# Kernel tuning notes

Measured on AMD Instinct MI355X. Metric: run time of the kernel, lower is better.

## Reference

```python
import jax, jax.numpy as jnp
import numpy as np

HIDDEN = 2048
SEL = 512
RES = HIDDEN - SEL
YSZ = 2048
RANK = 64
EPS = 1e-5


def _layernorm(x, gamma, beta):
    mu = jnp.mean(x, axis=-1, keepdims=True)
    var = jnp.mean(jnp.square(x - mu), axis=-1, keepdims=True)
    return (x - mu) * jax.lax.rsqrt(var + EPS) * gamma + beta


def setup_inputs() -> dict:
    key = jax.random.key(0)
    ks = jax.random.split(key, 8)
    B, S = 4, 4096
    hidden_states = jax.random.normal(ks[0], (B, S, HIDDEN), dtype=jnp.float32)
    y = jax.random.normal(ks[1], (B, S, YSZ), dtype=jnp.float32)
    A = -jnp.ones((1, 1, SEL), dtype=jnp.float32) + 0.02 * jax.random.normal(ks[2], (1, 1, SEL), dtype=jnp.float32)
    W_w = jax.random.normal(ks[3], (HIDDEN, YSZ), dtype=jnp.float32) * (1.0 / np.sqrt(YSZ))
    dd_w = jax.random.normal(ks[4], (RANK, HIDDEN + YSZ), dtype=jnp.float32) * (1.0 / np.sqrt(HIDDEN + YSZ))
    du_w = jax.random.normal(ks[5], (SEL, RANK), dtype=jnp.float32) * (1.0 / np.sqrt(RANK))
    t = 0.001 + jax.random.uniform(ks[6], (SEL,), dtype=jnp.float32) * (0.1 - 0.001)
    du_b = jnp.log(jnp.expm1(t))
    sel_gamma = jnp.ones((SEL,), dtype=jnp.float32)
    sel_beta = jnp.zeros((SEL,), dtype=jnp.float32)
    res_gamma = jnp.ones((RES,), dtype=jnp.float32)
    res_beta = jnp.zeros((RES,), dtype=jnp.float32)
    return {"hidden_states": hidden_states, "y": y, "A": A, "W_w": W_w,
            "dd_w": dd_w, "du_w": du_w, "du_b": du_b,
            "sel_gamma": sel_gamma, "sel_beta": sel_beta,
            "res_gamma": res_gamma, "res_beta": res_beta}


def reference(hidden_states, y, A, W_w, dd_w, du_w, du_b,
              sel_gamma, sel_beta, res_gamma, res_beta):
    sel_h = hidden_states[..., :SEL]
    res_h = hidden_states[..., SEL:]
    # W(y) split
    wy = jnp.einsum('bsy,hy->bsh', y, W_w)
    sel_y, res_y = wy[..., :SEL], wy[..., SEL:]
    # split layernorm of hidden_states
    normed = jnp.concatenate([
        _layernorm(sel_h, sel_gamma, sel_beta),
        _layernorm(res_h, res_gamma, res_beta)], axis=-1)
    # low-rank delta path
    cat = jnp.concatenate([normed, y], axis=-1)  # [B,S,HIDDEN+YSZ]
    low = jnp.einsum('bsc,rc->bsr', cat, dd_w)   # [B,S,RANK]
    delta = jnp.einsum('bsr,dr->bsd', low, du_w) + du_b  # [B,S,SEL]
    delta = jax.nn.softplus(delta)
    A_neg = -jax.nn.softplus(A)                  # [1,1,SEL]
    A_bar = jnp.exp(delta * A_neg)
    B_bar = (A_bar - 1.0) / A_neg
    sel_out = A_bar * sel_h + B_bar * sel_y
    res_out = res_h + res_y
    return jnp.concatenate([sel_out, res_out], axis=-1)
```

## Files before the change

### kernel.cpp

```cpp
#include <hip/hip_runtime.h>
#include <hip/hip_bf16.h>
#include <stdint.h>

#define NTOK   16384
#define HID    2048
#define SELN   512
#define RESN   1536
#define YSZn   2048
#define RANKn  64
#define EPSf   1e-5f

typedef __bf16 bf16x8 __attribute__((ext_vector_type(8)));
typedef float f32x4 __attribute__((ext_vector_type(4)));

__device__ __forceinline__ unsigned short f2bf(float f) {
  unsigned u = __float_as_uint(f);
  u += 0x7fff + ((u >> 16) & 1);
  return (unsigned short)(u >> 16);
}
__device__ __forceinline__ float bf2f(unsigned short h) {
  return __uint_as_float(((unsigned)h) << 16);
}
__device__ __forceinline__ float softplus_f(float x) {
  return fmaxf(x, 0.f) + log1pf(expf(-fabsf(x)));
}

#define GLD16(gp, lp) __builtin_amdgcn_global_load_lds( \
    (const __attribute__((address_space(1))) void*)(gp), \
    (__attribute__((address_space(3))) void*)(lp), 16, 0, 0)

#define CY (NTOK * HID / 8)
#define CW (HID * YSZn / 8)
#define CD (RANKn * (HID + YSZn) / 8)
__global__ __launch_bounds__(256) void k_convert(
    const float* __restrict__ y, const float* __restrict__ Ww,
    const float* __restrict__ ddw,
    unsigned short* __restrict__ ybf, unsigned short* __restrict__ wbf,
    unsigned short* __restrict__ dbf) {
  int64_t stride = (int64_t)gridDim.x * blockDim.x;
  for (int64_t i = (int64_t)blockIdx.x * blockDim.x + threadIdx.x;
       i < CY + CW + CD; i += stride) {
    const float* src; unsigned short* dst;
    if (i < CY)            { src = y   + i * 8;            dst = ybf + i * 8; }
    else if (i < CY + CW)  { int64_t j = i - CY;       src = Ww  + j * 8; dst = wbf + j * 8; }
    else                   { int64_t j = i - CY - CW;  src = ddw + j * 8; dst = dbf + j * 8; }
    float4 a = ((const float4*)src)[0];
    float4 b = ((const float4*)src)[1];
    union { unsigned short u[8]; uint4 q; } o;
    o.u[0]=f2bf(a.x); o.u[1]=f2bf(a.y); o.u[2]=f2bf(a.z); o.u[3]=f2bf(a.w);
    o.u[4]=f2bf(b.x); o.u[5]=f2bf(b.y); o.u[6]=f2bf(b.z); o.u[7]=f2bf(b.w);
    *(uint4*)dst = o.q;
  }
}

__global__ __launch_bounds__(256) void k_gemm_wy(
    const unsigned short* __restrict__ Y,
    const unsigned short* __restrict__ W,
    unsigned short* __restrict__ wy) {
  __shared__ unsigned short As[128 * 32];
  __shared__ unsigned short Bs[128 * 32];
  int bid = blockIdx.x;
  int swz = (bid & 7) * 256 + (bid >> 3);
  int mt = swz & 127, nt = swz >> 7;
  int m0 = mt * 128, n0 = nt * 128;
  int tid = threadIdx.x, w = tid >> 6, l = tid & 63;
  int wr = w >> 1, wc = w & 1;
  f32x4 acc[4][4] = {};

  int off0 = w * 1024 + l * 16;
  int r0 = off0 >> 6, kb0 = off0 & 63;
  int off1 = off0 + 4096;
  int r1 = off1 >> 6, kb1 = off1 & 63;
  const char* Ab = (const char*)Y;
  const char* Bb = (const char*)W;

  for (int kt = 0; kt < 64; ++kt) {
    int k0 = kt * 32;
    GLD16(Ab + ((size_t)(m0 + r0) * HID + k0) * 2 + kb0, (char*)As + w * 1024);
    GLD16(Ab + ((size_t)(m0 + r1) * HID + k0) * 2 + kb1, (char*)As + w * 1024 + 4096);
    GLD16(Bb + ((size_t)(n0 + r0) * HID + k0) * 2 + kb0, (char*)Bs + w * 1024);
    GLD16(Bb + ((size_t)(n0 + r1) * HID + k0) * 2 + kb1, (char*)Bs + w * 1024 + 4096);
    __syncthreads();
    bf16x8 af[4], bv[4];
    #pragma unroll
    for (int mi = 0; mi < 4; ++mi) {
      int row = wr * 64 + mi * 16 + (l & 15);
      af[mi] = *reinterpret_cast<const bf16x8*>(&As[row * 32 + ((l >> 4) * 8)]);
    }
    #pragma unroll
    for (int ni = 0; ni < 4; ++ni) {
      int row = wc * 64 + ni * 16 + (l & 15);
      bv[ni] = *reinterpret_cast<const bf16x8*>(&Bs[row * 32 + ((l >> 4) * 8)]);
    }
    #pragma unroll
    for (int mi = 0; mi < 4; ++mi)
      #pragma unroll
      for (int ni = 0; ni < 4; ++ni)
        acc[mi][ni] = __builtin_amdgcn_mfma_f32_16x16x32_bf16(af[mi], bv[ni], acc[mi][ni], 0, 0, 0);
    if (kt < 63) __syncthreads();
  }
  #pragma unroll
  for (int mi = 0; mi < 4; ++mi)
    #pragma unroll
    for (int ni = 0; ni < 4; ++ni) {
      int row = m0 + wr * 64 + mi * 16 + ((l >> 4) * 4);
      int col = n0 + wc * 64 + ni * 16 + (l & 15);
      #pragma unroll
      for (int rg = 0; rg < 4; ++rg)
        wy[(size_t)(row + rg) * HID + col] = f2bf(acc[mi][ni][rg]);
    }
}

__global__ __launch_bounds__(256) void k_ln(
    const float* __restrict__ hidden,
    const float* __restrict__ sg, const float* __restrict__ sb,
    const float* __restrict__ rg, const float* __restrict__ rb,
    unsigned short* __restrict__ normed) {
  int tok = blockIdx.x, tid = threadIdx.x;
  const float* x = hidden + (size_t)tok * HID;
  float4 a = ((const float4*)x)[tid * 2];
  float4 b = ((const float4*)x)[tid * 2 + 1];
  float v[8] = {a.x, a.y, a.z, a.w, b.x, b.y, b.z, b.w};
  float s = 0.f, ss = 0.f;
  #pragma unroll
  for (int j = 0; j < 8; ++j) { s += v[j]; ss += v[j] * v[j]; }
  #pragma unroll
  for (int off = 32; off > 0; off >>= 1) {
    s  += __shfl_xor(s, off);
    ss += __shfl_xor(ss, off);
  }
  __shared__ float ps[4], pss[4];
  int w = tid >> 6;
  if ((tid & 63) == 0) { ps[w] = s; pss[w] = ss; }
  __syncthreads();
  float mu, rstd; const float* gam; const float* bet; int cb;
  if (tid < 64) {
    float S = ps[0], SS = pss[0];
    mu = S * (1.f / 512.f);
    rstd = rsqrtf(SS * (1.f / 512.f) - mu * mu + EPSf);
    gam = sg; bet = sb; cb = tid * 8;
  } else {
    float S = ps[1] + ps[2] + ps[3], SS = pss[1] + pss[2] + pss[3];
    mu = S * (1.f / 1536.f);
    rstd = rsqrtf(SS * (1.f / 1536.f) - mu * mu + EPSf);
    gam = rg; bet = rb; cb = tid * 8 - 512;
  }
  union { unsigned short u[8]; uint4 q; } o;
  #pragma unroll
  for (int j = 0; j < 8; ++j)
    o.u[j] = f2bf((v[j] - mu) * rstd * gam[cb + j] + bet[cb + j]);
  *(uint4*)&normed[(size_t)tok * HID + tid * 8] = o.q;
}

__global__ __launch_bounds__(256) void k_gemm_low(
    const unsigned short* __restrict__ normed,
    const unsigned short* __restrict__ ybf,
    const unsigned short* __restrict__ ddw,
    float* __restrict__ low) {
  __shared__ unsigned short As[64 * 64];
  __shared__ unsigned short Bs[64 * 64];
  int m0 = blockIdx.x * 64;
  int tid = threadIdx.x, w = tid >> 6, l = tid & 63;
  f32x4 acc[4] = {};
  int off0 = w * 1024 + l * 16;
  int r0 = off0 >> 7, kb0 = off0 & 127;
  int off1 = off0 + 4096;
  int r1 = off1 >> 7, kb1 = off1 & 127;

  for (int kt = 0; kt < 64; ++kt) {
    const char* Asrc = (const char*)((kt < 32) ? normed : ybf);
    int k0 = (kt & 31) * 64;
    GLD16(Asrc + ((size_t)(m0 + r0) * HID + k0) * 2 + kb0, (char*)As + w * 1024);
    GLD16(Asrc + ((size_t)(m0 + r1) * HID + k0) * 2 + kb1, (char*)As + w * 1024 + 4096);
    GLD16((const char*)ddw + ((size_t)r0 * 4096 + kt * 64) * 2 + kb0, (char*)Bs + w * 1024);
    GLD16((const char*)ddw + ((size_t)r1 * 4096 + kt * 64) * 2 + kb1, (char*)Bs + w * 1024 + 4096);
    __syncthreads();
    #pragma unroll
    for (int kk = 0; kk < 2; ++kk) {
      bf16x8 af = *reinterpret_cast<const bf16x8*>(
          &As[(w * 16 + (l & 15)) * 64 + kk * 32 + (l >> 4) * 8]);
      #pragma unroll
      for (int ni = 0; ni < 4; ++ni) {
        bf16x8 bv = *reinterpret_cast<const bf16x8*>(
            &Bs[(ni * 16 + (l & 15)) * 64 + kk * 32 + (l >> 4) * 8]);
        acc[ni] = __builtin_amdgcn_mfma_f32_16x16x32_bf16(af, bv, acc[ni], 0, 0, 0);
      }
    }
    if (kt < 63) __syncthreads();
  }
  #pragma unroll
  for (int ni = 0; ni < 4; ++ni) {
    int row = m0 + w * 16 + ((l >> 4) * 4);
    int col = ni * 16 + (l & 15);
    #pragma unroll
    for (int rg = 0; rg < 4; ++rg)
      low[(size_t)(row + rg) * 64 + col] = acc[ni][rg];
  }
}

__global__ __launch_bounds__(512) void k_final(
    const float* __restrict__ hidden,
    const unsigned short* __restrict__ wy,
    const float* __restrict__ low,
    const float* __restrict__ A,
    const float* __restrict__ duw,
    const float* __restrict__ dub,
    float* __restrict__ out) {
  __shared__ float slow[8][64];
  int t0 = blockIdx.x * 8;
  int tid = threadIdx.x;
  slow[tid >> 6][tid & 63] = low[(size_t)t0 * 64 + tid];
  __syncthreads();

  int d = tid;
  float aneg = -softplus_f(A[d]);
  float dubv = dub[d];
  float wrow[64];
  #pragma unroll
  for (int r4 = 0; r4 < 16; ++r4) {
    float4 t = *(const float4*)&duw[(size_t)d * 64 + r4 * 4];
    wrow[r4 * 4 + 0] = t.x; wrow[r4 * 4 + 1] = t.y;
    wrow[r4 * 4 + 2] = t.z; wrow[r4 * 4 + 3] = t.w;
  }
  #pragma unroll 1
  for (int tk = 0; tk < 8; ++tk) {
    float acc = dubv;
    #pragma unroll
    for (int r = 0; r < 64; ++r) acc += wrow[r] * slow[tk][r];
    float delta = softplus_f(acc);
    float abar = expf(delta * aneg);
    float bbar = (abar - 1.f) / aneg;
    size_t base = (size_t)(t0 + tk) * HID;
    float selh = hidden[base + d];
    float sely = bf2f(wy[base + d]);
    out[base + d] = abar * selh + bbar * sely;
  }
  for (int i = tid; i < 8 * 384; i += 512) {
    int tk = i / 384, j = i - tk * 384;
    size_t base = (size_t)(t0 + tk) * HID + 512 + (size_t)j * 4;
    float4 h4 = *(const float4*)&hidden[base];
    ushort4 w4 = *(const ushort4*)&wy[base];
    float4 o;
    o.x = h4.x + bf2f(w4.x);
    o.y = h4.y + bf2f(w4.y);
    o.z = h4.z + bf2f(w4.z);
    o.w = h4.w + bf2f(w4.w);
    *(float4*)&out[base] = o;
  }
}

extern "C" void kernel_launch(void* const* d_in, const int* in_sizes, int n_in,
                              void* d_out, int out_size, void* d_ws, size_t ws_size,
                              hipStream_t stream) {
  (void)in_sizes; (void)n_in; (void)out_size; (void)ws_size;
  const float* hidden = (const float*)d_in[0];
  const float* y      = (const float*)d_in[1];
  const float* A      = (const float*)d_in[2];
  const float* Ww     = (const float*)d_in[3];
  const float* ddw    = (const float*)d_in[4];
  const float* duw    = (const float*)d_in[5];
  const float* dub    = (const float*)d_in[6];
  const float* sg     = (const float*)d_in[7];
  const float* sb     = (const float*)d_in[8];
  const float* rg     = (const float*)d_in[9];
  const float* rb     = (const float*)d_in[10];
  float* out = (float*)d_out;
  char* ws = (char*)d_ws;
  unsigned short* ybf  = (unsigned short*)(ws);
  unsigned short* wbf  = (unsigned short*)(ws + 67108864);
  unsigned short* dbf  = (unsigned short*)(ws + 75497472);
  unsigned short* wybf = (unsigned short*)(ws + 76021760);
  unsigned short* nrm  = (unsigned short*)(ws + 143130624);
  float*          low  = (float*)(ws + 210239488);

  hipLaunchKernelGGL(k_convert,  dim3(2048),  dim3(256), 0, stream, y, Ww, ddw, ybf, wbf, dbf);
  hipLaunchKernelGGL(k_gemm_wy,  dim3(2048),  dim3(256), 0, stream, ybf, wbf, wybf);
  hipLaunchKernelGGL(k_ln,       dim3(16384), dim3(256), 0, stream, hidden, sg, sb, rg, rb, nrm);
  hipLaunchKernelGGL(k_gemm_low, dim3(256),   dim3(256), 0, stream, nrm, ybf, dbf, low);
  hipLaunchKernelGGL(k_final,    dim3(2048),  dim3(512), 0, stream, hidden, wybf, low, A, duw, dub, out);
}
```

Before: 691.3 us.

## Rewrite wy GEMM with 256x256 double-buffered tiles and fused residual epilogue

Replaces the main W(y) GEMM with 256x256 tiles on 512 threads, a 128KB double-buffered LDS pipeline with swizzled layout, explicit waitcnt/barrier scheduling and setprio around MFMA clusters. The residual half (columns 512+) is written directly as hidden + wy in fp32 in the GEMM epilogue, so only the selective 512 columns are stored as bf16. This removes the full bf16 wy round-trip and the residual pass in k_final. The low-rank GEMM also gets swizzled double-buffered staging. The cost is large LDS usage per block, which limits occupancy, plus subtle manual vmcnt accounting.

```diff
diff --git a/kernel.cpp b/kernel.cpp
--- a/kernel.cpp
+++ b/kernel.cpp
@@ -5,9 +5,7 @@
 #define NTOK   16384
 #define HID    2048
 #define SELN   512
-#define RESN   1536
 #define YSZn   2048
-#define RANKn  64
 #define EPSf   1e-5f
 
 typedef __bf16 bf16x8 __attribute__((ext_vector_type(8)));
@@ -28,10 +26,13 @@
 #define GLD16(gp, lp) __builtin_amdgcn_global_load_lds( \
     (const __attribute__((address_space(1))) void*)(gp), \
     (__attribute__((address_space(3))) void*)(lp), 16, 0, 0)
+#define BAR()  __builtin_amdgcn_s_barrier()
+#define PRIO1() __builtin_amdgcn_s_setprio(1)
+#define PRIO0() __builtin_amdgcn_s_setprio(0)
 
 #define CY (NTOK * HID / 8)
 #define CW (HID * YSZn / 8)
-#define CD (RANKn * (HID + YSZn) / 8)
+#define CD (64 * (HID + YSZn) / 8)
 __global__ __launch_bounds__(256) void k_convert(
     const float* __restrict__ y, const float* __restrict__ Ww,
     const float* __restrict__ ddw,
@@ -53,62 +54,163 @@
   }
 }
 
-__global__ __launch_bounds__(256) void k_gemm_wy(
+__global__ __launch_bounds__(512, 2) void k_gemm_wy(
     const unsigned short* __restrict__ Y,
     const unsigned short* __restrict__ W,
-    unsigned short* __restrict__ wy) {
-  __shared__ unsigned short As[128 * 32];
-  __shared__ unsigned short Bs[128 * 32];
+    const float* __restrict__ hidden,
+    unsigned short* __restrict__ wysel,
+    float* __restrict__ out) {
+  __shared__ char lds[131072];
   int bid = blockIdx.x;
-  int swz = (bid & 7) * 256 + (bid >> 3);
-  int mt = swz & 127, nt = swz >> 7;
-  int m0 = mt * 128, n0 = nt * 128;
-  int tid = threadIdx.x, w = tid >> 6, l = tid & 63;
-  int wr = w >> 1, wc = w & 1;
-  f32x4 acc[4][4] = {};
-
-  int off0 = w * 1024 + l * 16;
-  int r0 = off0 >> 6, kb0 = off0 & 63;
-  int off1 = off0 + 4096;
-  int r1 = off1 >> 6, kb1 = off1 & 63;
-  const char* Ab = (const char*)Y;
-  const char* Bb = (const char*)W;
-
-  for (int kt = 0; kt < 64; ++kt) {
-    int k0 = kt * 32;
-    GLD16(Ab + ((size_t)(m0 + r0) * HID + k0) * 2 + kb0, (char*)As + w * 1024);
-    GLD16(Ab + ((size_t)(m0 + r1) * HID + k0) * 2 + kb1, (char*)As + w * 1024 + 4096);
-    GLD16(Bb + ((size_t)(n0 + r0) * HID + k0) * 2 + kb0, (char*)Bs + w * 1024);
-    GLD16(Bb + ((size_t)(n0 + r1) * HID + k0) * 2 + kb1, (char*)Bs + w * 1024 + 4096);
-    __syncthreads();
+  int nt = bid & 7, mt = bid >> 3;
+  int m0 = mt * 256, n0 = nt * 256;
+  int tid = threadIdx.x;
+  int l = tid & 63, w = tid >> 6;
+  int wr = w >> 2, wc = w & 3;
+
+  int rowS[2], colS[2];
+  #pragma unroll
+  for (int i = 0; i < 2; ++i) {
+    int L  = i * 8192 + tid * 16;
+    int rb = L >> 10;
+    int b  = L & 1023;
+    int rr = (b >> 6) & 15;
+    int cb = (b & 63) ^ ((rr >> 3) << 5);
+    rowS[i] = rb * 16 + rr;
+    colS[i] = cb >> 1;
+  }
+  const unsigned short* aSrc0 = Y + (size_t)(m0 + rowS[0]) * HID + colS[0];
+  const unsigned short* aSrc1 = Y + (size_t)(m0 + rowS[1]) * HID + colS[1];
+  const unsigned short* bSrc0 = W + (size_t)(n0 + rowS[0]) * HID + colS[0];
+  const unsigned short* bSrc1 = W + (size_t)(n0 + rowS[1]) * HID + colS[1];
+
+  int inner = (((l & 15) * 64) + ((l >> 4) * 16)) ^ (((l >> 3) & 1) << 5);
+  const char* ldsp = (const char*)lds;
+
+  f32x4 acc[8][4] = {};
+
+#define STAGE_A(kt, kh, bb) do { \
+    GLD16(aSrc0 + (size_t)(kt) * 64 + (kh) * 32, lds + (bb) + (kh) * 16384 + w * 1024); \
+    GLD16(aSrc1 + (size_t)(kt) * 64 + (kh) * 32, lds + (bb) + (kh) * 16384 + 8192 + w * 1024); \
+  } while (0)
+#define STAGE_B(kt, kh, bb) do { \
+    GLD16(bSrc0 + (size_t)(kt) * 64 + (kh) * 32, lds + 65536 + (bb) + (kh) * 16384 + w * 1024); \
+    GLD16(bSrc1 + (size_t)(kt) * 64 + (kh) * 32, lds + 65536 + (bb) + (kh) * 16384 + 8192 + w * 1024); \
+  } while (0)
+
+  auto rdA = [&](int cbase, int kk, int mg, bf16x8* af) {
+    #pragma unroll
+    for (int mi = 0; mi < 4; ++mi)
+      af[mi] = *(const bf16x8*)(ldsp + cbase + kk * 16384 +
+                                (mg * 8 + wr * 4 + mi) * 1024 + inner);
+  };
+  auto rdB = [&](int cbase, int kk, bf16x8* bv) {
+    #pragma unroll
+    for (int ni = 0; ni < 4; ++ni)
+      bv[ni] = *(const bf16x8*)(ldsp + 65536 + cbase + kk * 16384 +
+                                (wc * 4 + ni) * 1024 + inner);
+  };
+
+  STAGE_A(0, 0, 0); STAGE_B(0, 0, 0); STAGE_A(0, 1, 0); STAGE_B(0, 1, 0);
+  asm volatile("s_waitcnt vmcnt(4)");
+  BAR();
+
+  int buf = 0;
+  for (int kt = 0; kt < 32; ++kt) {
+    int cb = buf * 32768;
+    int sb = 32768 - cb;
+    bool last = (kt == 31);
     bf16x8 af[4], bv[4];
-    #pragma unroll
-    for (int mi = 0; mi < 4; ++mi) {
-      int row = wr * 64 + mi * 16 + (l & 15);
-      af[mi] = *reinterpret_cast<const bf16x8*>(&As[row * 32 + ((l >> 4) * 8)]);
-    }
-    #pragma unroll
-    for (int ni = 0; ni < 4; ++ni) {
-      int row = wc * 64 + ni * 16 + (l & 15);
-      bv[ni] = *reinterpret_cast<const bf16x8*>(&Bs[row * 32 + ((l >> 4) * 8)]);
-    }
+
+    rdA(cb, 0, 0, af); rdB(cb, 0, bv);
+    if (!last) STAGE_A(kt + 1, 0, sb);
+    BAR();
+    asm volatile("s_waitcnt lgkmcnt(0)");
+    PRIO1();
     #pragma unroll
     for (int mi = 0; mi < 4; ++mi)
       #pragma unroll
       for (int ni = 0; ni < 4; ++ni)
         acc[mi][ni] = __builtin_amdgcn_mfma_f32_16x16x32_bf16(af[mi], bv[ni], acc[mi][ni], 0, 0, 0);
-    if (kt < 63) __syncthreads();
-  }
-  #pragma unroll
-  for (int mi = 0; mi < 4; ++mi)
-    #pragma unroll
-    for (int ni = 0; ni < 4; ++ni) {
-      int row = m0 + wr * 64 + mi * 16 + ((l >> 4) * 4);
-      int col = n0 + wc * 64 + ni * 16 + (l & 15);
-      #pragma unroll
-      for (int rg = 0; rg < 4; ++rg)
-        wy[(size_t)(row + rg) * HID + col] = f2bf(acc[mi][ni][rg]);
-    }
+    PRIO0();
+    BAR();
+
+    rdA(cb, 0, 1, af);
+    if (!last) STAGE_B(kt + 1, 0, sb);
+    BAR();
+    asm volatile("s_waitcnt lgkmcnt(0)");
+    PRIO1();
+    #pragma unroll
+    for (int mi = 0; mi < 4; ++mi)
+      #pragma unroll
+      for (int ni = 0; ni < 4; ++ni)
+        acc[4 + mi][ni] = __builtin_amdgcn_mfma_f32_16x16x32_bf16(af[mi], bv[ni], acc[4 + mi][ni], 0, 0, 0);
+    PRIO0();
+    if (last) asm volatile("s_waitcnt vmcnt(0)");
+    else      asm volatile("s_waitcnt vmcnt(4)");
+    BAR();
+
+    rdA(cb, 1, 0, af); rdB(cb, 1, bv);
+    if (!last) STAGE_A(kt + 1, 1, sb);
+    BAR();
+    asm volatile("s_waitcnt lgkmcnt(0)");
+    PRIO1();
+    #pragma unroll
+    for (int mi = 0; mi < 4; ++mi)
+      #pragma unroll
+      for (int ni = 0; ni < 4; ++ni)
+        acc[mi][ni] = __builtin_amdgcn_mfma_f32_16x16x32_bf16(af[mi], bv[ni], acc[mi][ni], 0, 0, 0);
+    PRIO0();
+    BAR();
+
+    rdA(cb, 1, 1, af);
+    if (!last) STAGE_B(kt + 1, 1, sb);
+    BAR();
+    asm volatile("s_waitcnt lgkmcnt(0)");
+    PRIO1();
+    #pragma unroll
+    for (int mi = 0; mi < 4; ++mi)
+      #pragma unroll
+      for (int ni = 0; ni < 4; ++ni)
+        acc[4 + mi][ni] = __builtin_amdgcn_mfma_f32_16x16x32_bf16(af[mi], bv[ni], acc[4 + mi][ni], 0, 0, 0);
+    PRIO0();
+    if (!last) asm volatile("s_waitcnt vmcnt(4)");
+    BAR();
+
+    buf ^= 1;
+  }
+
+  if (nt < 2) {
+    #pragma unroll
+    for (int mg = 0; mg < 2; ++mg)
+      #pragma unroll
+      for (int mi = 0; mi < 4; ++mi)
+        #pragma unroll
+        for (int ni = 0; ni < 4; ++ni) {
+          int row = m0 + mg * 128 + wr * 64 + mi * 16 + ((l >> 4) * 4);
+          int col = n0 + wc * 64 + ni * 16 + (l & 15);
+          #pragma unroll
+          for (int rg = 0; rg < 4; ++rg)
+            wysel[(size_t)(row + rg) * SELN + col] = f2bf(acc[mg * 4 + mi][ni][rg]);
+        }
+  } else {
+    #pragma unroll
+    for (int mg = 0; mg < 2; ++mg)
+      #pragma unroll
+      for (int mi = 0; mi < 4; ++mi)
+        #pragma unroll
+        for (int ni = 0; ni < 4; ++ni) {
+          int row = m0 + mg * 128 + wr * 64 + mi * 16 + ((l >> 4) * 4);
+          int col = n0 + wc * 64 + ni * 16 + (l & 15);
+          #pragma unroll
+          for (int rg = 0; rg < 4; ++rg) {
+            size_t idx = (size_t)(row + rg) * HID + col;
+            out[idx] = hidden[idx] + acc[mg * 4 + mi][ni][rg];
+          }
+        }
+  }
+#undef STAGE_A
+#undef STAGE_B
 }
 
 __global__ __launch_bounds__(256) void k_ln(
@@ -157,36 +259,54 @@
     const unsigned short* __restrict__ ybf,
     const unsigned short* __restrict__ ddw,
     float* __restrict__ low) {
-  __shared__ unsigned short As[64 * 64];
-  __shared__ unsigned short Bs[64 * 64];
+  __shared__ char lds[32768];
   int m0 = blockIdx.x * 64;
   int tid = threadIdx.x, w = tid >> 6, l = tid & 63;
   f32x4 acc[4] = {};
-  int off0 = w * 1024 + l * 16;
-  int r0 = off0 >> 7, kb0 = off0 & 127;
-  int off1 = off0 + 4096;
-  int r1 = off1 >> 7, kb1 = off1 & 127;
-
+
+  int rowS[2], colS[2];
+  #pragma unroll
+  for (int i = 0; i < 2; ++i) {
+    int L  = i * 4096 + tid * 16;
+    int sbt = L >> 10;
+    int b  = L & 1023;
+    int rr = (b >> 6) & 15;
+    rowS[i] = (sbt >> 1) * 16 + rr;
+    colS[i] = (sbt & 1) * 32 + (((b & 63) ^ ((rr >> 3) << 5)) >> 1);
+  }
+  int inner = (((l & 15) * 64) + ((l >> 4) * 16)) ^ (((l >> 3) & 1) << 5);
+  const char* ldsp = (const char*)lds;
+
+  auto stage = [&](const unsigned short* As_, int kt, int bb) {
+    int k0 = (kt & 31) * 64;
+    GLD16(As_ + (size_t)(m0 + rowS[0]) * HID + k0 + colS[0], lds + bb + w * 1024);
+    GLD16(As_ + (size_t)(m0 + rowS[1]) * HID + k0 + colS[1], lds + bb + 4096 + w * 1024);
+    GLD16(ddw + (size_t)rowS[0] * 4096 + kt * 64 + colS[0], lds + bb + 8192 + w * 1024);
+    GLD16(ddw + (size_t)rowS[1] * 4096 + kt * 64 + colS[1], lds + bb + 8192 + 4096 + w * 1024);
+  };
+
+  stage(normed, 0, 0);
+  asm volatile("s_waitcnt vmcnt(0)");
+  BAR();
+  int buf = 0;
   for (int kt = 0; kt < 64; ++kt) {
-    const char* Asrc = (const char*)((kt < 32) ? normed : ybf);
-    int k0 = (kt & 31) * 64;
-    GLD16(Asrc + ((size_t)(m0 + r0) * HID + k0) * 2 + kb0, (char*)As + w * 1024);
-    GLD16(Asrc + ((size_t)(m0 + r1) * HID + k0) * 2 + kb1, (char*)As + w * 1024 + 4096);
-    GLD16((const char*)ddw + ((size_t)r0 * 4096 + kt * 64) * 2 + kb0, (char*)Bs + w * 1024);
-    GLD16((const char*)ddw + ((size_t)r1 * 4096 + kt * 64) * 2 + kb1, (char*)Bs + w * 1024 + 4096);
-    __syncthreads();
-    #pragma unroll
-    for (int kk = 0; kk < 2; ++kk) {
-      bf16x8 af = *reinterpret_cast<const bf16x8*>(
-          &As[(w * 16 + (l & 15)) * 64 + kk * 32 + (l >> 4) * 8]);
-      #pragma unroll
-      for (int ni = 0; ni < 4; ++ni) {
-        bf16x8 bv = *reinterpret_cast<const bf16x8*>(
-            &Bs[(ni * 16 + (l & 15)) * 64 + kk * 32 + (l >> 4) * 8]);
-        acc[ni] = __builtin_amdgcn_mfma_f32_16x16x32_bf16(af, bv, acc[ni], 0, 0, 0);
-      }
+    int cb = buf * 16384, sb = 16384 - cb;
+    if (kt < 63) stage((kt + 1 < 32) ? normed : ybf, kt + 1, sb);
+    bf16x8 af0 = *(const bf16x8*)(ldsp + cb + (w * 2 + 0) * 1024 + inner);
+    bf16x8 af1 = *(const bf16x8*)(ldsp + cb + (w * 2 + 1) * 1024 + inner);
+    #pragma unroll
+    for (int ni = 0; ni < 4; ++ni) {
+      bf16x8 b0 = *(const bf16x8*)(ldsp + cb + 8192 + (ni * 2 + 0) * 1024 + inner);
+      acc[ni] = __builtin_amdgcn_mfma_f32_16x16x32_bf16(af0, b0, acc[ni], 0, 0, 0);
     }
-    if (kt < 63) __syncthreads();
+    #pragma unroll
+    for (int ni = 0; ni < 4; ++ni) {
+      bf16x8 b1 = *(const bf16x8*)(ldsp + cb + 8192 + (ni * 2 + 1) * 1024 + inner);
+      acc[ni] = __builtin_amdgcn_mfma_f32_16x16x32_bf16(af1, b1, acc[ni], 0, 0, 0);
+    }
+    if (kt < 63) asm volatile("s_waitcnt vmcnt(0)");
+    BAR();
+    buf ^= 1;
   }
   #pragma unroll
   for (int ni = 0; ni < 4; ++ni) {
@@ -200,7 +320,7 @@
 
 __global__ __launch_bounds__(512) void k_final(
     const float* __restrict__ hidden,
-    const unsigned short* __restrict__ wy,
+    const unsigned short* __restrict__ wysel,
     const float* __restrict__ low,
     const float* __restrict__ A,
     const float* __restrict__ duw,
@@ -230,22 +350,10 @@
     float delta = softplus_f(acc);
     float abar = expf(delta * aneg);
     float bbar = (abar - 1.f) / aneg;
-    size_t base = (size_t)(t0 + tk) * HID;
-    float selh = hidden[base + d];
-    float sely = bf2f(wy[base + d]);
-    out[base + d] = abar * selh + bbar * sely;
-  }
-  for (int i = tid; i < 8 * 384; i += 512) {
-    int tk = i / 384, j = i - tk * 384;
-    size_t base = (size_t)(t0 + tk) * HID + 512 + (size_t)j * 4;
-    float4 h4 = *(const float4*)&hidden[base];
-    ushort4 w4 = *(const ushort4*)&wy[base];
-    float4 o;
-    o.x = h4.x + bf2f(w4.x);
-    o.y = h4.y + bf2f(w4.y);
-    o.z = h4.z + bf2f(w4.z);
-    o.w = h4.w + bf2f(w4.w);
-    *(float4*)&out[base] = o;
+    size_t tokb = (size_t)(t0 + tk);
+    float selh = hidden[tokb * HID + d];
+    float sely = bf2f(wysel[tokb * SELN + d]);
+    out[tokb * HID + d] = abar * selh + bbar * sely;
   }
 }
 
@@ -266,16 +374,16 @@
   const float* rb     = (const float*)d_in[10];
   float* out = (float*)d_out;
   char* ws = (char*)d_ws;
-  unsigned short* ybf  = (unsigned short*)(ws);
-  unsigned short* wbf  = (unsigned short*)(ws + 67108864);
-  unsigned short* dbf  = (unsigned short*)(ws + 75497472);
-  unsigned short* wybf = (unsigned short*)(ws + 76021760);
-  unsigned short* nrm  = (unsigned short*)(ws + 143130624);
-  float*          low  = (float*)(ws + 210239488);
+  unsigned short* ybf   = (unsigned short*)(ws);
+  unsigned short* wbf   = (unsigned short*)(ws + 67108864);
+  unsigned short* dbf   = (unsigned short*)(ws + 75497472);
+  unsigned short* wysel = (unsigned short*)(ws + 76021760);
+  unsigned short* nrm   = (unsigned short*)(ws + 92798976);
+  float*          low   = (float*)(ws + 159907840);
 
   hipLaunchKernelGGL(k_convert,  dim3(2048),  dim3(256), 0, stream, y, Ww, ddw, ybf, wbf, dbf);
-  hipLaunchKernelGGL(k_gemm_wy,  dim3(2048),  dim3(256), 0, stream, ybf, wbf, wybf);
+  hipLaunchKernelGGL(k_gemm_wy,  dim3(512),   dim3(512), 0, stream, ybf, wbf, hidden, wysel, out);
   hipLaunchKernelGGL(k_ln,       dim3(16384), dim3(256), 0, stream, hidden, sg, sb, rg, rb, nrm);
   hipLaunchKernelGGL(k_gemm_low, dim3(256),   dim3(256), 0, stream, nrm, ybf, dbf, low);
-  hipLaunchKernelGGL(k_final,    dim3(2048),  dim3(512), 0, stream, hidden, wybf, low, A, duw, dub, out);
-}
+  hipLaunchKernelGGL(k_final,    dim3(2048),  dim3(512), 0, stream, hidden, wysel, low, A, duw, dub, out);
+}
```

New measurement: 631.0 us. 8.7% less time.
